# Performance work log

Hardware: AMD Instinct MI355X
Metric: run time of the kernel (lower is better)

The kernel has to match this reference:

```python
import math
import jax, jax.numpy as jnp
import numpy as np

H = 256      # hidden_size
HEADS = 8
DK = H // HEADS
B = 32
DL = 290     # drug length
PL = 1000    # protein length


def _pe(length, d):
    # sinusoidal positional encoding, d even
    pos = jnp.arange(length, dtype=jnp.float32)[:, None]
    div = jnp.exp(jnp.arange(0, d, 2, dtype=jnp.float32) * (-math.log(10000.0) / d))
    ang = pos * div  # [L, d/2]
    pe = jnp.zeros((length, d), jnp.float32)
    pe = pe.at[:, 0::2].set(jnp.sin(ang)).at[:, 1::2].set(jnp.cos(ang))
    return pe


def setup_inputs() -> dict:
    key = jax.random.key(0)
    ks = iter(jax.random.split(key, 48))
    def lin(din, dout):
        return jax.random.normal(next(ks), (din, dout), jnp.float32) * 0.02, jnp.zeros((dout,), jnp.float32)
    inp = {}
    inp['drug'] = jax.random.normal(next(ks), (B, DL, H), jnp.float32)
    inp['protein'] = jax.random.normal(next(ks), (B, PL, H), jnp.float32)
    inp['scale_d'] = jnp.ones((1,), jnp.float32)
    inp['scale_p'] = jnp.ones((1,), jnp.float32)
    for name in ['q_d', 'k_p', 'v_p', 'q_p', 'k_d', 'v_d', 'out_d', 'out_p']:
        w, b = lin(H, H)
        inp['w_' + name] = w
        inp['b_' + name] = b
    inp['alpha'] = jnp.asarray(0.5, jnp.float32)
    for name in ['fc_dp', 'fc_pd']:
        w, b = lin(HEADS, H)
        inp['w_' + name] = w
        inp['b_' + name] = b
    for name in ['gd', 'gp']:
        w, b = lin(H, H)
        inp['w_' + name] = w
        inp['b_' + name] = b
    return inp


def _split_heads(x):
    b, l, _ = x.shape
    return x.reshape(b, l, HEADS, DK).transpose(0, 2, 1, 3)  # [b, h, l, dk]


def _forward(drug, protein, scale_d, scale_p,
             w_q_d, b_q_d, w_k_p, b_k_p, w_v_p, b_v_p,
             w_q_p, b_q_p, w_k_d, b_k_d, w_v_d, b_v_d,
             alpha, w_out_d, b_out_d, w_out_p, b_out_p,
             w_fc_dp, b_fc_dp, w_fc_pd, b_fc_pd,
             w_gd, b_gd, w_gp, b_gp):
    b, dl, h = drug.shape
    pl = protein.shape[1]
    # positional encoding (buffers, non-learned except scale)
    drug_e = drug + scale_d * _pe(dl, h)
    prot_e = protein + scale_p * _pe(pl, h)

    Qd = _split_heads(drug_e @ w_q_d + b_q_d)   # [b,h,dl,dk]
    Kp = _split_heads(prot_e @ w_k_p + b_k_p)   # [b,h,pl,dk]
    Vp = _split_heads(prot_e @ w_v_p + b_v_p)
    Qp = _split_heads(prot_e @ w_q_p + b_q_p)
    Kd = _split_heads(drug_e @ w_k_d + b_k_d)
    Vd = _split_heads(drug_e @ w_v_d + b_v_d)

    inv_sqrt = 1.0 / math.sqrt(DK)
    attn_dp = jnp.einsum('bhid,bhjd->bhij', Qd, Kp) * inv_sqrt      # [b,h,dl,pl]
    # (Q_p K_d^T)^T along last two dims -> [b,h,dl,pl]
    attn_pd = jnp.einsum('bhjd,bhid->bhij', Qp, Kd) * inv_sqrt
    a = jax.nn.sigmoid(alpha)
    A = jax.nn.softmax(a * attn_dp + (1.0 - a) * attn_pd, axis=-1)  # [b,h,dl,pl]

    ctx_d = jnp.einsum('bhij,bhjd->bhid', A, Vp)  # [b,h,dl,dk]
    ctx_p = jnp.einsum('bhij,bhid->bhjd', A, Vd)  # [b,h,pl,dk]
    ctx_d = ctx_d.transpose(0, 2, 1, 3).reshape(b, dl, h) @ w_out_d + b_out_d
    ctx_p = ctx_p.transpose(0, 2, 1, 3).reshape(b, pl, h) @ w_out_p + b_out_p

    attn_dp_m = jnp.mean(A, axis=-1).transpose(0, 2, 1)   # [b,dl,heads]
    drug_attn = attn_dp_m @ w_fc_dp + b_fc_dp             # [b,dl,h]
    attn_pd_m = jnp.mean(A, axis=-2).transpose(0, 2, 1)   # [b,pl,heads]
    prot_attn = attn_pd_m @ w_fc_pd + b_fc_pd             # [b,pl,h]

    drug_gate = jax.nn.sigmoid(drug_e @ w_gd + b_gd)
    prot_gate = jax.nn.sigmoid(prot_e @ w_gp + b_gp)
    ctx_d = ctx_d * drug_gate
    ctx_p = ctx_p * prot_gate

    drug_upd = drug_e + ctx_d * jax.nn.sigmoid(drug_attn)
    prot_upd = prot_e + ctx_p * jax.nn.sigmoid(prot_attn)
    return jnp.concatenate([drug_upd, prot_upd], axis=1)  # [b, dl+pl, h]


def reference(drug, protein, scale_d, scale_p,
              w_q_d, b_q_d, w_k_p, b_k_p, w_v_p, b_v_p,
              w_q_p, b_q_p, w_k_d, b_k_d, w_v_d, b_v_d,
              alpha, w_out_d, b_out_d, w_out_p, b_out_p,
              w_fc_dp, b_fc_dp, w_fc_pd, b_fc_pd,
              w_gd, b_gd, w_gp, b_gp):
    return _forward(drug, protein, scale_d, scale_p,
                    w_q_d, b_q_d, w_k_p, b_k_p, w_v_p, b_v_p,
                    w_q_p, b_q_p, w_k_d, b_k_d, w_v_d, b_v_d,
                    alpha, w_out_d, b_out_d, w_out_p, b_out_p,
                    w_fc_dp, b_fc_dp, w_fc_pd, b_fc_pd,
                    w_gd, b_gd, w_gp, b_gp)
```

## Files before the change

kernel.cpp:

```cpp
#include <hip/hip_runtime.h>
#include <math.h>

typedef __attribute__((ext_vector_type(8))) short bf16x8;
typedef __attribute__((ext_vector_type(4))) float f32x4;
typedef unsigned short u16;
typedef unsigned int u32;

#define DEVFN static __device__ __forceinline__

constexpr int NB  = 32;
constexpr int DLn = 290;
constexpr int PLc = 1000;
constexpr int MD  = NB * DLn;
constexpr int MP  = NB * PLc;
constexpr int NSTRIP = 645;
constexpr int SPLIT  = 145;

DEVFN u16 f2b(float f) {
    u32 u = __builtin_bit_cast(u32, f);
    u32 r = u + 0x7fffu + ((u >> 16) & 1u);
    return (u16)(r >> 16);
}
DEVFN float b2f(u16 s) { return __builtin_bit_cast(float, (u32)s << 16); }
DEVFN float sigm(float x) { return 1.0f / (1.0f + __expf(-x)); }
DEVFN int sw(int row, int col, int stride) { return row * stride + (col ^ ((row & 7) << 3)); }

__global__ void pe_kernel(float* __restrict__ pe) {
    int p = blockIdx.x, c = threadIdx.x;
    float div = __expf((float)(c & ~1) * (-9.210340371976184f / 256.0f));
    float ang = (float)p * div;
    pe[p * 256 + c] = (c & 1) ? cosf(ang) : sinf(ang);
}

struct WPtrs { const float* w[10]; };
__global__ __launch_bounds__(256) void wprep_kernel(WPtrs wp, u16* __restrict__ wt) {
    __shared__ u16 t[64][66];
    int m = blockIdx.y, tile = blockIdx.x;
    int k0 = (tile >> 2) * 64, n0 = (tile & 3) * 64;
    const float* w = wp.w[m];
    int r = threadIdx.x >> 6, c = threadIdx.x & 63;
    #pragma unroll
    for (int q = 0; q < 16; q++) {
        int rr = r + q * 4;
        t[rr][c] = f2b(w[(size_t)(k0 + rr) * 256 + n0 + c]);
    }
    __syncthreads();
    #pragma unroll
    for (int q = 0; q < 16; q++) {
        int rr = r + q * 4;
        wt[((size_t)m << 16) + (size_t)(n0 + rr) * 256 + k0 + c] = t[c][rr];
    }
}

struct PM { const u16* BT; const float* bias; u16* C; int sig; };
struct PCfg {
    const u16* Ab;
    const float* Af32;
    const float* scale;
    const float* pe;
    int plen;
    PM m[4];
};
struct PCfg2 { PCfg c0, c1; };

DEVFN void stageB(const u16* __restrict__ BT, int c, u16* dst0, int tid) {
    const int sub = tid >> 5;
    const int c32 = tid & 31;
    #pragma unroll
    for (int k = 0; k < 8; k++) {
        const int r = k * 8 + sub;
        const int nur = ((r >> 5) & 1) * 32 + ((r >> 2) & 3) * 8 + ((r >> 4) & 1) * 4 + (r & 3);
        const int kcol = ((c32 ^ (r & 7)) << 3);
        const u16* src = BT + (size_t)(c * 64 + nur) * 256 + kcol;
        u16* dst = dst0 + k * 2048 + tid * 8;
        __builtin_amdgcn_global_load_lds(
            (const __attribute__((address_space(1))) void*)src,
            (__attribute__((address_space(3))) void*)dst, 16, 0, 0);
    }
}

template<int NM>
__global__ __launch_bounds__(256) void proj_kernel(PCfg2 cfgs) {
    const int d = blockIdx.x;
    const int x = d & 7, q = d >> 3;
    const int j = q & 3, sg = q >> 2;
    const int s = sg * 8 + x;
    if (s >= NSTRIP) return;
    const bool f1 = s < SPLIT;
    const int mt = f1 ? s : s - SPLIT;

    const u16*   Ab    = f1 ? cfgs.c0.Ab    : cfgs.c1.Ab;
    const float* Af32  = f1 ? cfgs.c0.Af32  : cfgs.c1.Af32;
    const float* scale = f1 ? cfgs.c0.scale : cfgs.c1.scale;
    const float* pe    = f1 ? cfgs.c0.pe    : cfgs.c1.pe;
    const int    plen  = f1 ? cfgs.c0.plen  : cfgs.c1.plen;
    const int mi = (NM == 4) ? j : 0;
    const u16*   BT   = f1 ? (mi==0?cfgs.c0.m[0].BT  :mi==1?cfgs.c0.m[1].BT  :mi==2?cfgs.c0.m[2].BT  :cfgs.c0.m[3].BT)
                           : (mi==0?cfgs.c1.m[0].BT  :mi==1?cfgs.c1.m[1].BT  :mi==2?cfgs.c1.m[2].BT  :cfgs.c1.m[3].BT);
    const float* bias = f1 ? (mi==0?cfgs.c0.m[0].bias:mi==1?cfgs.c0.m[1].bias:mi==2?cfgs.c0.m[2].bias:cfgs.c0.m[3].bias)
                           : (mi==0?cfgs.c1.m[0].bias:mi==1?cfgs.c1.m[1].bias:mi==2?cfgs.c1.m[2].bias:cfgs.c1.m[3].bias);
    u16*         C    = f1 ? (mi==0?cfgs.c0.m[0].C   :mi==1?cfgs.c0.m[1].C   :mi==2?cfgs.c0.m[2].C   :cfgs.c0.m[3].C)
                           : (mi==0?cfgs.c1.m[0].C   :mi==1?cfgs.c1.m[1].C   :mi==2?cfgs.c1.m[2].C   :cfgs.c1.m[3].C);
    const int    sig  = f1 ? (mi==0?cfgs.c0.m[0].sig :mi==1?cfgs.c0.m[1].sig :mi==2?cfgs.c0.m[2].sig :cfgs.c0.m[3].sig)
                           : (mi==0?cfgs.c1.m[0].sig :mi==1?cfgs.c1.m[1].sig :mi==2?cfgs.c1.m[2].sig :cfgs.c1.m[3].sig);

    __shared__ u16 Bs[(NM == 4) ? 2 : 1][64 * 256];
    const int tid = threadIdx.x;
    const int lane = tid & 63, w = tid >> 6, ln = lane & 15, g = lane >> 4;

    stageB(BT, (NM == 4) ? 0 : j, &Bs[0][0], tid);

    bf16x8 Af[8];
    {
        const int row = mt * 64 + w * 16 + ln;
        if (Af32) {
            const int i = row % plen;
            const float sc = scale[0];
            const float* Xp_ = Af32 + (size_t)row * 256 + g * 8;
            const float* Pe_ = pe + (size_t)i * 256 + g * 8;
            #pragma unroll
            for (int ks = 0; ks < 8; ks++) {
                float4 xa = *(const float4*)(Xp_ + ks * 32);
                float4 xb = *(const float4*)(Xp_ + ks * 32 + 4);
                float4 pa = *(const float4*)(Pe_ + ks * 32);
                float4 pb = *(const float4*)(Pe_ + ks * 32 + 4);
                u16 o[8];
                o[0] = f2b(xa.x + sc * pa.x); o[1] = f2b(xa.y + sc * pa.y);
                o[2] = f2b(xa.z + sc * pa.z); o[3] = f2b(xa.w + sc * pa.w);
                o[4] = f2b(xb.x + sc * pb.x); o[5] = f2b(xb.y + sc * pb.y);
                o[6] = f2b(xb.z + sc * pb.z); o[7] = f2b(xb.w + sc * pb.w);
                Af[ks] = *(bf16x8*)o;
            }
        } else {
            const u16* Ap = Ab + (size_t)row * 256 + g * 8;
            #pragma unroll
            for (int ks = 0; ks < 8; ks++)
                Af[ks] = *(const bf16x8*)(Ap + ks * 32);
        }
    }
    asm volatile("s_waitcnt vmcnt(0)" ::: "memory");
    __syncthreads();

    #pragma unroll
    for (int c = 0; c < ((NM == 4) ? 4 : 1); c++) {
        const int cur = (NM == 4) ? (c & 1) : 0;
        const int chunk = (NM == 4) ? c : j;
        if (NM == 4 && c < 3) stageB(BT, c + 1, &Bs[(c + 1) & 1][0], tid);
        f32x4 acc[4] = {};
        #pragma unroll
        for (int ks = 0; ks < 8; ks++) {
            #pragma unroll
            for (int nt = 0; nt < 4; nt++) {
                bf16x8 bf = *(const bf16x8*)&Bs[cur][sw(nt * 16 + ln, ks * 32 + g * 8, 256)];
                acc[nt] = __builtin_amdgcn_mfma_f32_16x16x32_bf16(bf, Af[ks], acc[nt], 0, 0, 0);
            }
        }
        {
            const int row = mt * 64 + w * 16 + ln;
            const int base0 = chunk * 64 + g * 8, base1 = base0 + 32;
            f32x4 b0 = *(const f32x4*)&bias[base0];
            f32x4 b1 = *(const f32x4*)&bias[base0 + 4];
            f32x4 b2 = *(const f32x4*)&bias[base1];
            f32x4 b3 = *(const f32x4*)&bias[base1 + 4];
            float v[16];
            #pragma unroll
            for (int t = 0; t < 4; t++) {
                v[t]      = acc[0][t] + b0[t];
                v[4 + t]  = acc[1][t] + b1[t];
                v[8 + t]  = acc[2][t] + b2[t];
                v[12 + t] = acc[3][t] + b3[t];
            }
            if (sig) {
                #pragma unroll
                for (int t = 0; t < 16; t++) v[t] = sigm(v[t]);
            }
            u16 o[16];
            #pragma unroll
            for (int t = 0; t < 16; t++) o[t] = f2b(v[t]);
            u16* Cp = C + (size_t)row * 256;
            *(uint4*)&Cp[base0] = *(uint4*)&o[0];
            *(uint4*)&Cp[base1] = *(uint4*)&o[8];
        }
        if (NM == 4 && c < 3) {
            asm volatile("s_waitcnt vmcnt(0)" ::: "memory");
            __syncthreads();
        }
    }
}

__global__ __launch_bounds__(512) void attn_kernel(
        const u16* __restrict__ Qd, const u16* __restrict__ Kd, const u16* __restrict__ Vd,
        const u16* __restrict__ Kp, const u16* __restrict__ Vp, const u16* __restrict__ Qp,
        const float* __restrict__ alpha,
        u16* __restrict__ ctx_d, u16* __restrict__ ctx_p, float* __restrict__ cm) {
    __shared__ u16 Ks[2][64 * 64];
    __shared__ union {
        struct { u16 VpT[2][32 * 64]; u16 Pm[320 * 64]; } s1;
        struct { u16 PT[64 * 320]; u16 VdT[32 * 320]; } s2;
    } U;
    __shared__ float r_l[320];
    __shared__ float colpart[8][64];

    const int bh = blockIdx.x, b = bh >> 3, h = bh & 7;
    const int tid = threadIdx.x;
    const int w = tid >> 6, lane = tid & 63, ln = lane & 15, g = lane >> 4;

    const float a = sigm(alpha[0]);
    const float inv = 0.1767766952966369f;
    const float sa = a * inv, sb = (1.0f - a) * inv;
    const int nmt = (w < 4) ? 3 : 2;
    const int mtsA[3] = { w, w + 8, w + 16 };

    const size_t rbd = (size_t)b * DLn * 256 + h * 32;
    const size_t rbp = (size_t)b * PLc * 256 + h * 32;

    bf16x8 Qf[3][2];
    #pragma unroll
    for (int t = 0; t < 3; t++) {
        const int i = mtsA[t] * 16 + ln;
        #pragma unroll
        for (int ks = 0; ks < 2; ks++) {
            u16 o[8] = {0,0,0,0,0,0,0,0};
            if (t < nmt && i < DLn) {
                const u16* src = (ks ? Kd : Qd) + rbd + (size_t)i * 256 + g * 8;
                const float s = ks ? sb : sa;
                uint4 v = *(const uint4*)src;
                u16 e[8]; *(uint4*)e = v;
                #pragma unroll
                for (int q = 0; q < 8; q++) o[q] = f2b(b2f(e[q]) * s);
            }
            Qf[t][ks] = *(bf16x8*)o;
        }
    }

    const int s_jj = tid >> 3, s_ch = tid & 7;
    const u16* s_src = ((s_ch >> 2) ? Qp : Kp) + rbp + (s_ch & 3) * 8;
    const int v_j = tid & 63, v_d0 = (tid >> 6) * 4;

    {
        int j = s_jj;
        uint4 kv = (j < PLc) ? *(const uint4*)(s_src + (size_t)j * 256) : make_uint4(0,0,0,0);
        uint2 vv = (v_j < PLc) ? *(const uint2*)(Vp + rbp + (size_t)v_j * 256 + v_d0) : make_uint2(0,0);
        *(uint4*)&Ks[0][sw(s_jj, s_ch * 8, 64)] = kv;
        u16 e[4]; *(uint2*)e = vv;
        #pragma unroll
        for (int q = 0; q < 4; q++) U.s1.VpT[0][sw(v_d0 + q, v_j, 64)] = e[q];
    }
    __syncthreads();

    float rs[3] = {0.f, 0.f, 0.f};
    f32x4 accd[3][2] = {};
    for (int jt = 0; jt < 16; jt++) {
        const int cur = jt & 1, j0 = jt * 64;
        const int jn = j0 + 64 + s_jj;
        uint4 kv = (jn < PLc) ? *(const uint4*)(s_src + (size_t)jn * 256) : make_uint4(0,0,0,0);
        const int vn = j0 + 64 + v_j;
        uint2 vv = (vn < PLc) ? *(const uint2*)(Vp + rbp + (size_t)vn * 256 + v_d0) : make_uint2(0,0);

        bf16x8 kf[4][2];
        #pragma unroll
        for (int js = 0; js < 4; js++)
            #pragma unroll
            for (int ks = 0; ks < 2; ks++)
                kf[js][ks] = *(const bf16x8*)&Ks[cur][sw(js * 16 + ln, ks * 32 + g * 8, 64)];

        #pragma unroll
        for (int t = 0; t < 3; t++) {
            if (t >= nmt) break;
            const int mt = mtsA[t];
            f32x4 acc[4] = {};
            #pragma unroll
            for (int ks = 0; ks < 2; ks++)
                #pragma unroll
                for (int js = 0; js < 4; js++)
                    acc[js] = __builtin_amdgcn_mfma_f32_16x16x32_bf16(kf[js][ks], Qf[t][ks], acc[js], 0, 0, 0);
            const int irow = mt * 16 + ln;
            #pragma unroll
            for (int js = 0; js < 4; js++) {
                u16 pb[4];
                float psum = 0.f;
                #pragma unroll
                for (int r = 0; r < 4; r++) {
                    float p = __expf(acc[js][r]);
                    psum += p;
                    pb[r] = f2b(p);
                }
                rs[t] += psum;
                *(ushort4*)&U.s1.Pm[sw(irow, js * 16 + g * 4, 64)] = *(ushort4*)pb;
            }
        }
        #pragma unroll
        for (int t = 0; t < 3; t++) {
            if (t >= nmt) break;
            const int mt = mtsA[t];
            #pragma unroll
            for (int ks2 = 0; ks2 < 2; ks2++) {
                bf16x8 af = *(const bf16x8*)&U.s1.Pm[sw(mt * 16 + ln, ks2 * 32 + g * 8, 64)];
                #pragma unroll
                for (int nd = 0; nd < 2; nd++) {
                    bf16x8 bv = *(const bf16x8*)&U.s1.VpT[cur][sw(nd * 16 + ln, ks2 * 32 + g * 8, 64)];
                    accd[t][nd] = __builtin_amdgcn_mfma_f32_16x16x32_bf16(bv, af, accd[t][nd], 0, 0, 0);
                }
            }
        }
        *(uint4*)&Ks[cur ^ 1][sw(s_jj, s_ch * 8, 64)] = kv;
        {
            u16 e[4]; *(uint2*)e = vv;
            #pragma unroll
            for (int q = 0; q < 4; q++) U.s1.VpT[cur ^ 1][sw(v_d0 + q, v_j, 64)] = e[q];
        }
        __syncthreads();
    }

    #pragma unroll
    for (int t = 0; t < 3; t++) {
        float v = rs[t];
        v += __shfl_xor(v, 16);
        v += __shfl_xor(v, 32);
        rs[t] = v;
    }
    if (g == 0) {
        #pragma unroll
        for (int t = 0; t < 3; t++) {
            if (t >= nmt) break;
            const int i = mtsA[t] * 16 + ln;
            r_l[i] = (i < DLn) ? 1.0f / (rs[t] - 24.0f) : 0.0f;
        }
    }
    __syncthreads();

    #pragma unroll
    for (int t = 0; t < 3; t++) {
        if (t >= nmt) break;
        const int i = mtsA[t] * 16 + ln;
        if (i < DLn) {
            const float ri = r_l[i];
            #pragma unroll
            for (int nd = 0; nd < 2; nd++) {
                u16 o[4];
                #pragma unroll
                for (int r = 0; r < 4; r++) o[r] = f2b(accd[t][nd][r] * ri);
                *(uint2*)&ctx_d[rbd + (size_t)i * 256 + nd * 16 + g * 4] = *(uint2*)o;
            }
        }
    }
    for (int c = tid; c < 320 * 8; c += 512) {
        const int i = c >> 3, d0 = (c & 7) * 4;
        u16 o[4] = {0,0,0,0};
        if (i < DLn) {
            const float ri = r_l[i];
            uint2 v = *(const uint2*)(Vd + rbd + (size_t)i * 256 + d0);
            u16 e[4]; *(uint2*)e = v;
            #pragma unroll
            for (int q = 0; q < 4; q++) o[q] = f2b(b2f(e[q]) * ri);
        }
        #pragma unroll
        for (int q = 0; q < 4; q++) U.s2.VdT[sw(d0 + q, i, 320)] = o[q];
    }
    {
        int j = s_jj;
        uint4 kv = (j < PLc) ? *(const uint4*)(s_src + (size_t)j * 256) : make_uint4(0,0,0,0);
        *(uint4*)&Ks[0][sw(s_jj, s_ch * 8, 64)] = kv;
    }
    float rr[3][4];
    #pragma unroll
    for (int t = 0; t < 3; t++)
        #pragma unroll
        for (int r = 0; r < 4; r++)
            rr[t][r] = (t < nmt) ? r_l[mtsA[t] * 16 + g * 4 + r] : 0.0f;
    __syncthreads();

    for (int jt = 0; jt < 16; jt++) {
        const int cur = jt & 1, j0 = jt * 64;
        const int jn = j0 + 64 + s_jj;
        uint4 kv = (jn < PLc) ? *(const uint4*)(s_src + (size_t)jn * 256) : make_uint4(0,0,0,0);

        bf16x8 kf[4][2];
        #pragma unroll
        for (int js = 0; js < 4; js++)
            #pragma unroll
            for (int ks = 0; ks < 2; ks++)
                kf[js][ks] = *(const bf16x8*)&Ks[cur][sw(js * 16 + ln, ks * 32 + g * 8, 64)];

        float csl[4] = {0.f, 0.f, 0.f, 0.f};
        #pragma unroll
        for (int t = 0; t < 3; t++) {
            if (t >= nmt) break;
            const int mt = mtsA[t];
            f32x4 acc[4] = {};
            #pragma unroll
            for (int ks = 0; ks < 2; ks++)
                #pragma unroll
                for (int js = 0; js < 4; js++)
                    acc[js] = __builtin_amdgcn_mfma_f32_16x16x32_bf16(Qf[t][ks], kf[js][ks], acc[js], 0, 0, 0);
            #pragma unroll
            for (int js = 0; js < 4; js++) {
                u16 pb[4];
                #pragma unroll
                for (int r = 0; r < 4; r++) {
                    float p = __expf(acc[js][r]);
                    csl[js] += p * rr[t][r];
                    pb[r] = f2b(p);
                }
                *(ushort4*)&U.s2.PT[sw(js * 16 + ln, mt * 16 + g * 4, 320)] = *(ushort4*)pb;
            }
        }
        #pragma unroll
        for (int js = 0; js < 4; js++) {
            float v = csl[js];
            v += __shfl_xor(v, 16);
            v += __shfl_xor(v, 32);
            csl[js] = v;
        }
        if (g == 0) {
            #pragma unroll
            for (int js = 0; js < 4; js++) colpart[w][js * 16 + ln] = csl[js];
        }
        *(uint4*)&Ks[cur ^ 1][sw(s_jj, s_ch * 8, 64)] = kv;
        __syncthreads();

        {
            const int js2 = w & 3, ds2 = w >> 2;
            f32x4 ap = {};
            #pragma unroll
            for (int k = 0; k < 10; k++) {
                bf16x8 af = *(const bf16x8*)&U.s2.PT[sw(js2 * 16 + ln, k * 32 + g * 8, 320)];
                bf16x8 bv = *(const bf16x8*)&U.s2.VdT[sw(ds2 * 16 + ln, k * 32 + g * 8, 320)];
                ap = __builtin_amdgcn_mfma_f32_16x16x32_bf16(bv, af, ap, 0, 0, 0);
            }
            const int j = j0 + js2 * 16 + ln;
            if (j < PLc) {
                u16 o[4];
                #pragma unroll
                for (int r = 0; r < 4; r++) o[r] = f2b(ap[r]);
                *(uint2*)&ctx_p[rbp + (size_t)j * 256 + ds2 * 16 + g * 4] = *(uint2*)o;
            }
        }
        if (w == 0) {
            float tot = 0.f;
            #pragma unroll
            for (int ww = 0; ww < 8; ww++) tot += colpart[ww][lane];
            const int j = j0 + lane;
            if (j < PLc) cm[(size_t)(b * PLc + j) * 8 + h] = tot * (1.0f / 290.0f);
        }
        __syncthreads();
    }
}

__global__ __launch_bounds__(256) void combine_kernel(
        const float* __restrict__ drug, const float* __restrict__ prot,
        const float* __restrict__ scale_d, const float* __restrict__ scale_p,
        const float* __restrict__ pe,
        const u16* __restrict__ Xd, const u16* __restrict__ Xp,
        const u16* __restrict__ gate_d, const u16* __restrict__ gate_p,
        const float* __restrict__ cm,
        const float* __restrict__ w_fc_dp, const float* __restrict__ b_fc_dp,
        const float* __restrict__ w_fc_pd, const float* __restrict__ b_fc_pd,
        float* __restrict__ out) {
    int idx = blockIdx.x * 256 + threadIdx.x;
    int r = idx >> 6, c4 = (idx & 63) * 4;
    if (r < MD) {
        int b = r / DLn, i = r % DLn;
        float s = scale_d[0];
        float4 dv = *(const float4*)&drug[(size_t)r * 256 + c4];
        float4 pv = *(const float4*)&pe[i * 256 + c4];
        uint2 xv = *(const uint2*)&Xd[(size_t)r * 256 + c4];
        uint2 gv = *(const uint2*)&gate_d[(size_t)r * 256 + c4];
        float4 bb = *(const float4*)&b_fc_dp[c4];
        float da[4] = { bb.x, bb.y, bb.z, bb.w };
        #pragma unroll
        for (int hh = 0; hh < 8; hh++) {
            float4 wv = *(const float4*)&w_fc_dp[hh * 256 + c4];
            da[0] += 0.001f * wv.x; da[1] += 0.001f * wv.y;
            da[2] += 0.001f * wv.z; da[3] += 0.001f * wv.w;
        }
        u16 xe[4]; *(uint2*)xe = xv;
        u16 ge[4]; *(uint2*)ge = gv;
        float e0 = dv.x + s * pv.x, e1 = dv.y + s * pv.y;
        float e2 = dv.z + s * pv.z, e3 = dv.w + s * pv.w;
        float4 o;
        o.x = e0 + b2f(xe[0]) * b2f(ge[0]) * sigm(da[0]);
        o.y = e1 + b2f(xe[1]) * b2f(ge[1]) * sigm(da[1]);
        o.z = e2 + b2f(xe[2]) * b2f(ge[2]) * sigm(da[2]);
        o.w = e3 + b2f(xe[3]) * b2f(ge[3]) * sigm(da[3]);
        *(float4*)&out[((size_t)b * 1290 + i) * 256 + c4] = o;
    } else {
        int rr = r - MD;
        int b = rr / PLc, j = rr % PLc;
        float s = scale_p[0];
        float4 dv = *(const float4*)&prot[(size_t)rr * 256 + c4];
        float4 pv = *(const float4*)&pe[j * 256 + c4];
        uint2 xv = *(const uint2*)&Xp[(size_t)rr * 256 + c4];
        uint2 gv = *(const uint2*)&gate_p[(size_t)rr * 256 + c4];
        float4 bb = *(const float4*)&b_fc_pd[c4];
        float pa[4] = { bb.x, bb.y, bb.z, bb.w };
        #pragma unroll
        for (int hh = 0; hh < 8; hh++) {
            float cmh = cm[(size_t)rr * 8 + hh];
            float4 wv = *(const float4*)&w_fc_pd[hh * 256 + c4];
            pa[0] += cmh * wv.x; pa[1] += cmh * wv.y;
            pa[2] += cmh * wv.z; pa[3] += cmh * wv.w;
        }
        u16 xe[4]; *(uint2*)xe = xv;
        u16 ge[4]; *(uint2*)ge = gv;
        float e0 = dv.x + s * pv.x, e1 = dv.y + s * pv.y;
        float e2 = dv.z + s * pv.z, e3 = dv.w + s * pv.w;
        float4 o;
        o.x = e0 + b2f(xe[0]) * b2f(ge[0]) * sigm(pa[0]);
        o.y = e1 + b2f(xe[1]) * b2f(ge[1]) * sigm(pa[1]);
        o.z = e2 + b2f(xe[2]) * b2f(ge[2]) * sigm(pa[2]);
        o.w = e3 + b2f(xe[3]) * b2f(ge[3]) * sigm(pa[3]);
        *(float4*)&out[((size_t)b * 1290 + 290 + j) * 256 + c4] = o;
    }
}

extern "C" void kernel_launch(void* const* d_in, const int* in_sizes, int n_in,
                              void* d_out, int out_size, void* d_ws, size_t ws_size,
                              hipStream_t stream) {
    (void)in_sizes; (void)n_in; (void)out_size;
    const float* drug    = (const float*)d_in[0];
    const float* prot    = (const float*)d_in[1];
    const float* scale_d = (const float*)d_in[2];
    const float* scale_p = (const float*)d_in[3];

    char* ws = (char*)d_ws;
    size_t off = 0;
    auto alloc = [&](size_t bytes) -> void* {
        void* p = ws + off;
        off += (bytes + 255) & ~(size_t)255;
        return p;
    };
    float* pe   = (float*)alloc((size_t)1000 * 256 * 4);
    u16* wt     = (u16*)alloc((size_t)10 * 65536 * 2);
    u16* Qd     = (u16*)alloc((size_t)MD * 256 * 2);
    u16* Kd     = (u16*)alloc((size_t)MD * 256 * 2);
    u16* Vd     = (u16*)alloc((size_t)MD * 256 * 2);
    u16* gate_d = (u16*)alloc((size_t)MD * 256 * 2);
    u16* Kp     = (u16*)alloc((size_t)MP * 256 * 2);
    u16* Vp     = (u16*)alloc((size_t)MP * 256 * 2);
    u16* Qp     = (u16*)alloc((size_t)MP * 256 * 2);
    u16* gate_p = (u16*)alloc((size_t)MP * 256 * 2);
    u16* ctxd   = (u16*)alloc((size_t)MD * 256 * 2);
    u16* ctxp   = (u16*)alloc((size_t)MP * 256 * 2);
    float* cm   = (float*)alloc((size_t)MP * 8 * 4);
    u16* Xd     = (u16*)alloc((size_t)MD * 256 * 2);
    u16* Xp     = (u16*)alloc((size_t)MP * 256 * 2);
    if (off > ws_size) return;

    pe_kernel<<<1000, 256, 0, stream>>>(pe);

    WPtrs wp;
    const int wsrc[10] = {4, 12, 14, 25, 6, 8, 10, 27, 16, 18};
    for (int m = 0; m < 10; m++) wp.w[m] = (const float*)d_in[wsrc[m]];
    wprep_kernel<<<dim3(16, 10), 256, 0, stream>>>(wp, wt);

    auto W = [&](int slot) { return wt + (size_t)slot * 65536; };
    const int GRID = ((NSTRIP + 7) / 8) * 8 * 4;

    PCfg2 p1;
    p1.c0 = { nullptr, drug, scale_d, pe, DLn,
              { { W(0), (const float*)d_in[5],  Qd,     0 },
                { W(1), (const float*)d_in[13], Kd,     0 },
                { W(2), (const float*)d_in[15], Vd,     0 },
                { W(3), (const float*)d_in[26], gate_d, 1 } } };
    p1.c1 = { nullptr, prot, scale_p, pe, PLc,
              { { W(4), (const float*)d_in[7],  Kp,     0 },
                { W(5), (const float*)d_in[9],  Vp,     0 },
                { W(6), (const float*)d_in[11], Qp,     0 },
                { W(7), (const float*)d_in[28], gate_p, 1 } } };
    proj_kernel<4><<<GRID, 256, 0, stream>>>(p1);

    attn_kernel<<<256, 512, 0, stream>>>(Qd, Kd, Vd, Kp, Vp, Qp,
                                         (const float*)d_in[20], ctxd, ctxp, cm);

    PCfg2 p2;
    p2.c0 = { ctxd, nullptr, nullptr, nullptr, DLn,
              { { W(8), (const float*)d_in[17], Xd, 0 }, {}, {}, {} } };
    p2.c1 = { ctxp, nullptr, nullptr, nullptr, PLc,
              { { W(9), (const float*)d_in[19], Xp, 0 }, {}, {}, {} } };
    proj_kernel<1><<<GRID, 256, 0, stream>>>(p2);

    combine_kernel<<<(MD + MP) / 4, 256, 0, stream>>>(drug, prot, scale_d, scale_p, pe,
        Xd, Xp, gate_d, gate_p, cm,
        (const float*)d_in[21], (const float*)d_in[22],
        (const float*)d_in[23], (const float*)d_in[24],
        (float*)d_out);
}
```

Baseline: 204.0 us.

## Fuse combine epilogue into output projection and single-buffer weight staging

```diff
diff --git a/kernel.cpp b/kernel.cpp
--- a/kernel.cpp
+++ b/kernel.cpp
@@ -61,7 +61,15 @@
     int plen;
     PM m[4];
 };
-struct PCfg2 { PCfg c0, c1; };
+struct PCfg2 {
+    PCfg c0, c1;
+    const float* x0; const float* x1;
+    const u16* gate0; const u16* gate1;
+    const float* cm;
+    const float* wfc0; const float* bfc0;
+    const float* wfc1; const float* bfc1;
+    float* out;
+};
 
 DEVFN void stageB(const u16* __restrict__ BT, int c, u16* dst0, int tid) {
     const int sub = tid >> 5;
@@ -80,7 +88,7 @@
 }
 
 template<int NM>
-__global__ __launch_bounds__(256) void proj_kernel(PCfg2 cfgs) {
+__global__ __launch_bounds__(256, 4) void proj_kernel(PCfg2 cfgs) {
     const int d = blockIdx.x;
     const int x = d & 7, q = d >> 3;
     const int j = q & 3, sg = q >> 2;
@@ -93,7 +101,6 @@
     const float* Af32  = f1 ? cfgs.c0.Af32  : cfgs.c1.Af32;
     const float* scale = f1 ? cfgs.c0.scale : cfgs.c1.scale;
     const float* pe    = f1 ? cfgs.c0.pe    : cfgs.c1.pe;
-    const int    plen  = f1 ? cfgs.c0.plen  : cfgs.c1.plen;
     const int mi = (NM == 4) ? j : 0;
     const u16*   BT   = f1 ? (mi==0?cfgs.c0.m[0].BT  :mi==1?cfgs.c0.m[1].BT  :mi==2?cfgs.c0.m[2].BT  :cfgs.c0.m[3].BT)
                            : (mi==0?cfgs.c1.m[0].BT  :mi==1?cfgs.c1.m[1].BT  :mi==2?cfgs.c1.m[2].BT  :cfgs.c1.m[3].BT);
@@ -104,17 +111,17 @@
     const int    sig  = f1 ? (mi==0?cfgs.c0.m[0].sig :mi==1?cfgs.c0.m[1].sig :mi==2?cfgs.c0.m[2].sig :cfgs.c0.m[3].sig)
                            : (mi==0?cfgs.c1.m[0].sig :mi==1?cfgs.c1.m[1].sig :mi==2?cfgs.c1.m[2].sig :cfgs.c1.m[3].sig);
 
-    __shared__ u16 Bs[(NM == 4) ? 2 : 1][64 * 256];
+    __shared__ u16 Bs[64 * 256];
     const int tid = threadIdx.x;
     const int lane = tid & 63, w = tid >> 6, ln = lane & 15, g = lane >> 4;
 
-    stageB(BT, (NM == 4) ? 0 : j, &Bs[0][0], tid);
-
+    stageB(BT, (NM == 4) ? 0 : j, &Bs[0], tid);
+
+    const int row = mt * 64 + w * 16 + ln;
     bf16x8 Af[8];
     {
-        const int row = mt * 64 + w * 16 + ln;
         if (Af32) {
-            const int i = row % plen;
+            const int i = f1 ? (row % DLn) : (row % PLc);
             const float sc = scale[0];
             const float* Xp_ = Af32 + (size_t)row * 256 + g * 8;
             const float* Pe_ = pe + (size_t)i * 256 + g * 8;
@@ -143,33 +150,35 @@
 
     #pragma unroll
     for (int c = 0; c < ((NM == 4) ? 4 : 1); c++) {
-        const int cur = (NM == 4) ? (c & 1) : 0;
         const int chunk = (NM == 4) ? c : j;
-        if (NM == 4 && c < 3) stageB(BT, c + 1, &Bs[(c + 1) & 1][0], tid);
         f32x4 acc[4] = {};
         #pragma unroll
         for (int ks = 0; ks < 8; ks++) {
             #pragma unroll
             for (int nt = 0; nt < 4; nt++) {
-                bf16x8 bf = *(const bf16x8*)&Bs[cur][sw(nt * 16 + ln, ks * 32 + g * 8, 256)];
+                bf16x8 bf = *(const bf16x8*)&Bs[sw(nt * 16 + ln, ks * 32 + g * 8, 256)];
                 acc[nt] = __builtin_amdgcn_mfma_f32_16x16x32_bf16(bf, Af[ks], acc[nt], 0, 0, 0);
             }
         }
-        {
-            const int row = mt * 64 + w * 16 + ln;
-            const int base0 = chunk * 64 + g * 8, base1 = base0 + 32;
-            f32x4 b0 = *(const f32x4*)&bias[base0];
-            f32x4 b1 = *(const f32x4*)&bias[base0 + 4];
-            f32x4 b2 = *(const f32x4*)&bias[base1];
-            f32x4 b3 = *(const f32x4*)&bias[base1 + 4];
-            float v[16];
-            #pragma unroll
-            for (int t = 0; t < 4; t++) {
-                v[t]      = acc[0][t] + b0[t];
-                v[4 + t]  = acc[1][t] + b1[t];
-                v[8 + t]  = acc[2][t] + b2[t];
-                v[12 + t] = acc[3][t] + b3[t];
-            }
+        const bool hasNext = (NM == 4) && (c < 3);
+        if (hasNext) {
+            __syncthreads();
+            stageB(BT, c + 1, &Bs[0], tid);
+        }
+        const int base0 = chunk * 64 + g * 8, base1 = base0 + 32;
+        f32x4 b0 = *(const f32x4*)&bias[base0];
+        f32x4 b1 = *(const f32x4*)&bias[base0 + 4];
+        f32x4 b2 = *(const f32x4*)&bias[base1];
+        f32x4 b3 = *(const f32x4*)&bias[base1 + 4];
+        float v[16];
+        #pragma unroll
+        for (int t = 0; t < 4; t++) {
+            v[t]      = acc[0][t] + b0[t];
+            v[4 + t]  = acc[1][t] + b1[t];
+            v[8 + t]  = acc[2][t] + b2[t];
+            v[12 + t] = acc[3][t] + b3[t];
+        }
+        if (NM == 4) {
             if (sig) {
                 #pragma unroll
                 for (int t = 0; t < 16; t++) v[t] = sigm(v[t]);
@@ -180,8 +189,58 @@
             u16* Cp = C + (size_t)row * 256;
             *(uint4*)&Cp[base0] = *(uint4*)&o[0];
             *(uint4*)&Cp[base1] = *(uint4*)&o[8];
-        }
-        if (NM == 4 && c < 3) {
+        } else {
+            (void)C; (void)sig;
+            const float* X   = f1 ? cfgs.x0 : cfgs.x1;
+            const u16* gate  = f1 ? cfgs.gate0 : cfgs.gate1;
+            const float* wfc = f1 ? cfgs.wfc0 : cfgs.wfc1;
+            const float* bfc = f1 ? cfgs.bfc0 : cfgs.bfc1;
+            const float sc   = scale[0];
+            const int pos  = f1 ? (row % DLn) : (row % PLc);
+            const int bidx = f1 ? (row / DLn) : (row / PLc);
+            const int orow = f1 ? (bidx * 1290 + pos) : (bidx * 1290 + 290 + pos);
+            float cmv[8];
+            if (!f1) {
+                float4 ca = *(const float4*)&cfgs.cm[(size_t)row * 8];
+                float4 cb = *(const float4*)&cfgs.cm[(size_t)row * 8 + 4];
+                cmv[0]=ca.x; cmv[1]=ca.y; cmv[2]=ca.z; cmv[3]=ca.w;
+                cmv[4]=cb.x; cmv[5]=cb.y; cmv[6]=cb.z; cmv[7]=cb.w;
+            }
+            u16 ge[16];
+            *(uint4*)&ge[0] = *(const uint4*)&gate[(size_t)row * 256 + base0];
+            *(uint4*)&ge[8] = *(const uint4*)&gate[(size_t)row * 256 + base1];
+            float outv[16];
+            #pragma unroll
+            for (int half = 0; half < 2; half++) {
+                const int cb0 = half ? base1 : base0;
+                #pragma unroll
+                for (int t4 = 0; t4 < 2; t4++) {
+                    float4 xa = *(const float4*)&X[(size_t)row * 256 + cb0 + t4 * 4];
+                    float4 pa = *(const float4*)&pe[(size_t)pos * 256 + cb0 + t4 * 4];
+                    #pragma unroll
+                    for (int t = 0; t < 4; t++) {
+                        const int idx = half * 8 + t4 * 4 + t;
+                        const int col = cb0 + t4 * 4 + t;
+                        float aw = bfc[col];
+                        if (f1) {
+                            #pragma unroll
+                            for (int hh = 0; hh < 8; hh++) aw += 0.001f * wfc[hh * 256 + col];
+                        } else {
+                            #pragma unroll
+                            for (int hh = 0; hh < 8; hh++) aw += cmv[hh] * wfc[hh * 256 + col];
+                        }
+                        float e = (&xa.x)[t] + sc * (&pa.x)[t];
+                        outv[idx] = e + v[idx] * b2f(ge[idx]) * sigm(aw);
+                    }
+                }
+            }
+            float* Op = cfgs.out + (size_t)orow * 256;
+            *(float4*)&Op[base0]     = *(float4*)&outv[0];
+            *(float4*)&Op[base0 + 4] = *(float4*)&outv[4];
+            *(float4*)&Op[base1]     = *(float4*)&outv[8];
+            *(float4*)&Op[base1 + 4] = *(float4*)&outv[12];
+        }
+        if (hasNext) {
             asm volatile("s_waitcnt vmcnt(0)" ::: "memory");
             __syncthreads();
         }
@@ -444,73 +503,6 @@
             if (j < PLc) cm[(size_t)(b * PLc + j) * 8 + h] = tot * (1.0f / 290.0f);
         }
         __syncthreads();
-    }
-}
-
-__global__ __launch_bounds__(256) void combine_kernel(
-        const float* __restrict__ drug, const float* __restrict__ prot,
-        const float* __restrict__ scale_d, const float* __restrict__ scale_p,
-        const float* __restrict__ pe,
-        const u16* __restrict__ Xd, const u16* __restrict__ Xp,
-        const u16* __restrict__ gate_d, const u16* __restrict__ gate_p,
-        const float* __restrict__ cm,
-        const float* __restrict__ w_fc_dp, const float* __restrict__ b_fc_dp,
-        const float* __restrict__ w_fc_pd, const float* __restrict__ b_fc_pd,
-        float* __restrict__ out) {
-    int idx = blockIdx.x * 256 + threadIdx.x;
-    int r = idx >> 6, c4 = (idx & 63) * 4;
-    if (r < MD) {
-        int b = r / DLn, i = r % DLn;
-        float s = scale_d[0];
-        float4 dv = *(const float4*)&drug[(size_t)r * 256 + c4];
-        float4 pv = *(const float4*)&pe[i * 256 + c4];
-        uint2 xv = *(const uint2*)&Xd[(size_t)r * 256 + c4];
-        uint2 gv = *(const uint2*)&gate_d[(size_t)r * 256 + c4];
-        float4 bb = *(const float4*)&b_fc_dp[c4];
-        float da[4] = { bb.x, bb.y, bb.z, bb.w };
-        #pragma unroll
-        for (int hh = 0; hh < 8; hh++) {
-            float4 wv = *(const float4*)&w_fc_dp[hh * 256 + c4];
-            da[0] += 0.001f * wv.x; da[1] += 0.001f * wv.y;
-            da[2] += 0.001f * wv.z; da[3] += 0.001f * wv.w;
-        }
-        u16 xe[4]; *(uint2*)xe = xv;
-        u16 ge[4]; *(uint2*)ge = gv;
-        float e0 = dv.x + s * pv.x, e1 = dv.y + s * pv.y;
-        float e2 = dv.z + s * pv.z, e3 = dv.w + s * pv.w;
-        float4 o;
-        o.x = e0 + b2f(xe[0]) * b2f(ge[0]) * sigm(da[0]);
-        o.y = e1 + b2f(xe[1]) * b2f(ge[1]) * sigm(da[1]);
-        o.z = e2 + b2f(xe[2]) * b2f(ge[2]) * sigm(da[2]);
-        o.w = e3 + b2f(xe[3]) * b2f(ge[3]) * sigm(da[3]);
-        *(float4*)&out[((size_t)b * 1290 + i) * 256 + c4] = o;
-    } else {
-        int rr = r - MD;
-        int b = rr / PLc, j = rr % PLc;
-        float s = scale_p[0];
-        float4 dv = *(const float4*)&prot[(size_t)rr * 256 + c4];
-        float4 pv = *(const float4*)&pe[j * 256 + c4];
-        uint2 xv = *(const uint2*)&Xp[(size_t)rr * 256 + c4];
-        uint2 gv = *(const uint2*)&gate_p[(size_t)rr * 256 + c4];
-        float4 bb = *(const float4*)&b_fc_pd[c4];
-        float pa[4] = { bb.x, bb.y, bb.z, bb.w };
-        #pragma unroll
-        for (int hh = 0; hh < 8; hh++) {
-            float cmh = cm[(size_t)rr * 8 + hh];
-            float4 wv = *(const float4*)&w_fc_pd[hh * 256 + c4];
-            pa[0] += cmh * wv.x; pa[1] += cmh * wv.y;
-            pa[2] += cmh * wv.z; pa[3] += cmh * wv.w;
-        }
-        u16 xe[4]; *(uint2*)xe = xv;
-        u16 ge[4]; *(uint2*)ge = gv;
-        float e0 = dv.x + s * pv.x, e1 = dv.y + s * pv.y;
-        float e2 = dv.z + s * pv.z, e3 = dv.w + s * pv.w;
-        float4 o;
-        o.x = e0 + b2f(xe[0]) * b2f(ge[0]) * sigm(pa[0]);
-        o.y = e1 + b2f(xe[1]) * b2f(ge[1]) * sigm(pa[1]);
-        o.z = e2 + b2f(xe[2]) * b2f(ge[2]) * sigm(pa[2]);
-        o.w = e3 + b2f(xe[3]) * b2f(ge[3]) * sigm(pa[3]);
-        *(float4*)&out[((size_t)b * 1290 + 290 + j) * 256 + c4] = o;
     }
 }
 
@@ -543,8 +535,6 @@
     u16* ctxd   = (u16*)alloc((size_t)MD * 256 * 2);
     u16* ctxp   = (u16*)alloc((size_t)MP * 256 * 2);
     float* cm   = (float*)alloc((size_t)MP * 8 * 4);
-    u16* Xd     = (u16*)alloc((size_t)MD * 256 * 2);
-    u16* Xp     = (u16*)alloc((size_t)MP * 256 * 2);
     if (off > ws_size) return;
 
     pe_kernel<<<1000, 256, 0, stream>>>(pe);
@@ -557,7 +547,7 @@
     auto W = [&](int slot) { return wt + (size_t)slot * 65536; };
     const int GRID = ((NSTRIP + 7) / 8) * 8 * 4;
 
-    PCfg2 p1;
+    PCfg2 p1 = {};
     p1.c0 = { nullptr, drug, scale_d, pe, DLn,
               { { W(0), (const float*)d_in[5],  Qd,     0 },
                 { W(1), (const float*)d_in[13], Kd,     0 },
@@ -573,16 +563,16 @@
     attn_kernel<<<256, 512, 0, stream>>>(Qd, Kd, Vd, Kp, Vp, Qp,
                                          (const float*)d_in[20], ctxd, ctxp, cm);
 
-    PCfg2 p2;
-    p2.c0 = { ctxd, nullptr, nullptr, nullptr, DLn,
-              { { W(8), (const float*)d_in[17], Xd, 0 }, {}, {}, {} } };
-    p2.c1 = { ctxp, nullptr, nullptr, nullptr, PLc,
-              { { W(9), (const float*)d_in[19], Xp, 0 }, {}, {}, {} } };
+    PCfg2 p2 = {};
+    p2.c0 = { ctxd, nullptr, scale_d, pe, DLn,
+              { { W(8), (const float*)d_in[17], nullptr, 0 }, {}, {}, {} } };
+    p2.c1 = { ctxp, nullptr, scale_p, pe, PLc,
+              { { W(9), (const float*)d_in[19], nullptr, 0 }, {}, {}, {} } };
+    p2.x0 = drug;  p2.x1 = prot;
+    p2.gate0 = gate_d;  p2.gate1 = gate_p;
+    p2.cm = cm;
+    p2.wfc0 = (const float*)d_in[21];  p2.bfc0 = (const float*)d_in[22];
+    p2.wfc1 = (const float*)d_in[23];  p2.bfc1 = (const float*)d_in[24];
+    p2.out = (float*)d_out;
     proj_kernel<1><<<GRID, 256, 0, stream>>>(p2);
-
-    combine_kernel<<<(MD + MP) / 4, 256, 0, stream>>>(drug, prot, scale_d, scale_p, pe,
-        Xd, Xp, gate_d, gate_p, cm,
-        (const float*)d_in[21], (const float*)d_in[22],
-        (const float*)d_in[23], (const float*)d_in[24],
-        (float*)d_out);
-}
+}
```

Result: faster. 195.4 us (-4.2%).
